# Kernel tuning notes

Measured on AMD Instinct MI355X. Metric: run time of the kernel, lower is better.

## Reference

```python
import jax, jax.numpy as jnp
import numpy as np


def _morpho(x, weight, bias, sign, padding, stride):
    # x: [B,C,H,W], weight: [B,C,kh,kw], bias: [B,C], sign: [B]
    B, C, H, W = x.shape
    kh, kw = weight.shape[-2:]
    # sign handling: if |sign| >= 1e-7 multiply by sign, else leave unchanged
    m = (jnp.abs(sign) >= 1e-7).astype(x.dtype)          # [B], constant (detached in torch)
    s = m * sign + (1.0 - m)                              # effective multiplier per sample
    xs = x * s[:, None, None, None]
    # unfold zero-pads, and sign*0 == 0, so padding signed x with zeros is equivalent
    xp = jnp.pad(xs, ((0, 0), (0, 0), (padding, padding), (padding, padding)))
    H2 = (H + 2 * padding - kh) // stride + 1
    W2 = (W + 2 * padding - kw) // stride + 1
    # direct windowed max-plus: y[b,c,i,j] = max_{p,q} xs_pad[b,c,i*s+p,j*s+q] + w[b,c,p,q]
    # small fixed kh*kw loop avoids materializing the B*C*kh*kw*L unfold tensor
    y = jnp.full((B, C, H2, W2), -jnp.inf, dtype=x.dtype)
    for p in range(kh):
        for q in range(kw):
            patch = jax.lax.slice(
                xp,
                (0, 0, p, q),
                (B, C, p + (H2 - 1) * stride + 1, q + (W2 - 1) * stride + 1),
                (1, 1, stride, stride),
            )  # [B,C,H2,W2]
            y = jnp.maximum(y, patch + weight[:, :, p, q][:, :, None, None])
    y = y + bias[:, :, None, None]
    return y * s[:, None, None, None]


def setup_inputs() -> dict:
    key = jax.random.key(0)
    k1, k2, k3, k4 = jax.random.split(key, 4)
    B, C, H, W, kh, kw = 16, 64, 128, 128, 5, 5
    return {
        "x": jax.random.normal(k1, (B, C, H, W), dtype=jnp.float32),
        "weight": jax.random.normal(k2, (B, C, kh, kw), dtype=jnp.float32) * 0.1,
        "bias": jax.random.normal(k3, (B, C), dtype=jnp.float32) * 0.1,
        "sign": jax.random.normal(k4, (B,), dtype=jnp.float32),
        "padding": 2,
        "stride": 1,
    }


def reference(x, weight, bias, sign, padding, stride):
    return _morpho(x, weight, bias, sign, padding, stride)
```

## Files before the change

### kernel.cpp

```cpp
#include <hip/hip_runtime.h>
#include <math.h>
#include <stdint.h>

#define HH 128
#define WW 128
#define NFLOATS (16 * 64 * HH * WW)

typedef __fp16 h2 __attribute__((ext_vector_type(2)));

__device__ __forceinline__ h2 h2max(h2 a, h2 b) { return __builtin_elementwise_max(a, b); }
__device__ __forceinline__ uint32_t h2u(h2 v) { return __builtin_bit_cast(uint32_t, v); }
__device__ __forceinline__ h2 uh2(uint32_t v) { return __builtin_bit_cast(h2, v); }

#if __has_builtin(__builtin_elementwise_fma)
#define H2FMA(a, b, c) __builtin_elementwise_fma((a), (b), (c))
#else
#define H2FMA(a, b, c) ((a) * (b) + (c))
#endif

__global__ __launch_bounds__(256, 8) void morpho_kernel(
    const float* __restrict__ x,
    const float* __restrict__ wgt,
    const float* __restrict__ bias,
    const float* __restrict__ sign,
    float* __restrict__ out)
{
    const int bid  = blockIdx.x;
    const int blk  = (bid & 7) * 512 + (bid >> 3);
    const int quad = blk & 3;
    const int bc   = blk >> 2;
    const int b    = bc >> 6;

    float*       __restrict__ yp = out + (size_t)bc * (HH * WW);
    const float* __restrict__ wp = wgt + bc * 25;

    const float sgn = sign[b];
    const float s   = (fabsf(sgn) >= 1e-7f) ? sgn : 1.0f;
    const float bvs = bias[bc] * s;
    const __fp16 sh = (__fp16)s;
    const h2 s2 = { sh, sh };

    uint32_t wsu[25];
#pragma unroll
    for (int k = 0; k < 25; ++k) {
        const __fp16 wh = (__fp16)wp[k];
        h2 w2 = { wh, wh };
        wsu[k] = (uint32_t)__builtin_amdgcn_readfirstlane((int)h2u(w2));
    }

    const int t  = threadIdx.x;
    const int tx = t & 31;
    const int ty = t >> 5;
    const int j0 = tx * 4;
    const int i0 = quad * 32 + ty * 4;
    const int planeOff = bc * (HH * WW);

    const bool mL = (tx > 0);
    const bool mR = (tx < 31);

    h2 acc0[4], acc1[4];

#pragma unroll
    for (int r8 = 0; r8 < 8; ++r8) {
        const int  r  = i0 - 2 + r8;
        const bool rv = ((unsigned)r < (unsigned)HH);
        const int  rc = min(max(r, 0), HH - 1);
        const int  oM = planeOff + rc * WW + j0;
        const int  oL = max(oM - 4, 0);
        const int  oR = min(oM + 4, NFLOATS - 4);
        const float4 v0 = *reinterpret_cast<const float4*>(x + oL);
        const float4 v1 = *reinterpret_cast<const float4*>(x + oM);
        const float4 v2 = *reinterpret_cast<const float4*>(x + oR);

        uint32_t e0 = h2u(__builtin_amdgcn_cvt_pkrtz(v0.z, v0.w));
        uint32_t e1 = h2u(__builtin_amdgcn_cvt_pkrtz(v1.x, v1.y));
        uint32_t e2 = h2u(__builtin_amdgcn_cvt_pkrtz(v1.z, v1.w));
        uint32_t e3 = h2u(__builtin_amdgcn_cvt_pkrtz(v2.x, v2.y));
        e0 = (rv && mL) ? e0 : 0u;
        e1 = rv ? e1 : 0u;
        e2 = rv ? e2 : 0u;
        e3 = (rv && mR) ? e3 : 0u;
        const uint32_t o0 = __builtin_amdgcn_alignbit(e1, e0, 16);
        const uint32_t o1 = __builtin_amdgcn_alignbit(e2, e1, 16);
        const uint32_t o2 = __builtin_amdgcn_alignbit(e3, e2, 16);

        const uint32_t P0[5] = { e0, o0, e1, o1, e2 };
        const uint32_t P1[5] = { e1, o1, e2, o2, e3 };

#pragma unroll
        for (int p = 0; p < 5; ++p) {
            const int oi = r8 - p;
            if (oi >= 0 && oi < 4) {
                const h2 w0 = uh2(wsu[p * 5 + 0]);
                const h2 w1 = uh2(wsu[p * 5 + 1]);
                const h2 w2 = uh2(wsu[p * 5 + 2]);
                const h2 w3 = uh2(wsu[p * 5 + 3]);
                const h2 w4 = uh2(wsu[p * 5 + 4]);
                {
                    const h2 t0 = H2FMA(uh2(P0[0]), s2, w0);
                    const h2 t1 = H2FMA(uh2(P0[1]), s2, w1);
                    const h2 t2 = H2FMA(uh2(P0[2]), s2, w2);
                    const h2 t3 = H2FMA(uh2(P0[3]), s2, w3);
                    const h2 t4 = H2FMA(uh2(P0[4]), s2, w4);
                    h2 mm = h2max(h2max(h2max(t0, t1), h2max(t2, t3)), t4);
                    acc0[oi] = (p == 0) ? mm : h2max(acc0[oi], mm);
                }
                {
                    const h2 t0 = H2FMA(uh2(P1[0]), s2, w0);
                    const h2 t1 = H2FMA(uh2(P1[1]), s2, w1);
                    const h2 t2 = H2FMA(uh2(P1[2]), s2, w2);
                    const h2 t3 = H2FMA(uh2(P1[3]), s2, w3);
                    const h2 t4 = H2FMA(uh2(P1[4]), s2, w4);
                    h2 mm = h2max(h2max(h2max(t0, t1), h2max(t2, t3)), t4);
                    acc1[oi] = (p == 0) ? mm : h2max(acc1[oi], mm);
                }
            }
        }
    }

#pragma unroll
    for (int a = 0; a < 4; ++a) {
        float4 o;
        o.x = fmaf((float)acc0[a][0], s, bvs);
        o.y = fmaf((float)acc0[a][1], s, bvs);
        o.z = fmaf((float)acc1[a][0], s, bvs);
        o.w = fmaf((float)acc1[a][1], s, bvs);
        *reinterpret_cast<float4*>(yp + (size_t)(i0 + a) * WW + j0) = o;
    }
}

extern "C" void kernel_launch(void* const* d_in, const int* in_sizes, int n_in,
                              void* d_out, int out_size, void* d_ws, size_t ws_size,
                              hipStream_t stream) {
    (void)d_ws; (void)ws_size; (void)in_sizes; (void)n_in; (void)out_size;
    const float* x    = (const float*)d_in[0];
    const float* w    = (const float*)d_in[1];
    const float* bias = (const float*)d_in[2];
    const float* sign = (const float*)d_in[3];
    float* out = (float*)d_out;

    morpho_kernel<<<4096, 256, 0, stream>>>(x, w, bias, sign, out);
}
```

Baseline: 33.54 us.

## Software-pipeline row loads with inline asm and explicit vmcnt waits

Replaces the compiler-scheduled row loop with hand-issued inline-asm global loads, kept four rows ahead, and explicit s_waitcnt vmcnt waits with sched barriers between consume steps. This overlaps memory latency with the packed-half max-plus math. The left and right halo loads shrink from float4 to float2, cutting redundant bytes. The launch-bounds occupancy hint of 8 is also dropped, which frees register pressure for the in-flight buffers but may lower occupancy.

```diff
diff --git a/kernel.cpp b/kernel.cpp
--- a/kernel.cpp
+++ b/kernel.cpp
@@ -18,7 +18,10 @@
 #define H2FMA(a, b, c) ((a) * (b) + (c))
 #endif
 
-__global__ __launch_bounds__(256, 8) void morpho_kernel(
+#define WAITV(n) do { asm volatile("s_waitcnt vmcnt(" #n ")" ::: "memory"); \
+                      __builtin_amdgcn_sched_barrier(0); } while (0)
+
+__global__ __launch_bounds__(256) void morpho_kernel(
     const float* __restrict__ x,
     const float* __restrict__ wgt,
     const float* __restrict__ bias,
@@ -54,28 +57,30 @@
     const int j0 = tx * 4;
     const int i0 = quad * 32 + ty * 4;
     const int planeOff = bc * (HH * WW);
-
     const bool mL = (tx > 0);
     const bool mR = (tx < 31);
 
+    float2 vl[8]; float4 vm[8]; float2 vr[8];
     h2 acc0[4], acc1[4];
 
-#pragma unroll
-    for (int r8 = 0; r8 < 8; ++r8) {
-        const int  r  = i0 - 2 + r8;
-        const bool rv = ((unsigned)r < (unsigned)HH);
-        const int  rc = min(max(r, 0), HH - 1);
-        const int  oM = planeOff + rc * WW + j0;
-        const int  oL = max(oM - 4, 0);
-        const int  oR = min(oM + 4, NFLOATS - 4);
-        const float4 v0 = *reinterpret_cast<const float4*>(x + oL);
-        const float4 v1 = *reinterpret_cast<const float4*>(x + oM);
-        const float4 v2 = *reinterpret_cast<const float4*>(x + oR);
+    auto ISSUE = [&](int r8) {
+        const int rrow = i0 - 2 + r8;
+        const int rc = min(max(rrow, 0), HH - 1);
+        const int oM = planeOff + rc * WW + j0;
+        const int oL = max(oM - 2, 0);
+        const int oR = min(oM + 4, NFLOATS - 2);
+        asm volatile("global_load_dwordx2 %0, %1, off" : "=v"(vl[r8]) : "v"(x + oL));
+        asm volatile("global_load_dwordx4 %0, %1, off" : "=v"(vm[r8]) : "v"(x + oM));
+        asm volatile("global_load_dwordx2 %0, %1, off" : "=v"(vr[r8]) : "v"(x + oR));
+    };
 
-        uint32_t e0 = h2u(__builtin_amdgcn_cvt_pkrtz(v0.z, v0.w));
-        uint32_t e1 = h2u(__builtin_amdgcn_cvt_pkrtz(v1.x, v1.y));
-        uint32_t e2 = h2u(__builtin_amdgcn_cvt_pkrtz(v1.z, v1.w));
-        uint32_t e3 = h2u(__builtin_amdgcn_cvt_pkrtz(v2.x, v2.y));
+    auto CONSUME = [&](int r8) {
+        const int  rrow = i0 - 2 + r8;
+        const bool rv = ((unsigned)rrow < (unsigned)HH);
+        uint32_t e0 = h2u(__builtin_amdgcn_cvt_pkrtz(vl[r8].x, vl[r8].y));
+        uint32_t e1 = h2u(__builtin_amdgcn_cvt_pkrtz(vm[r8].x, vm[r8].y));
+        uint32_t e2 = h2u(__builtin_amdgcn_cvt_pkrtz(vm[r8].z, vm[r8].w));
+        uint32_t e3 = h2u(__builtin_amdgcn_cvt_pkrtz(vr[r8].x, vr[r8].y));
         e0 = (rv && mL) ? e0 : 0u;
         e1 = rv ? e1 : 0u;
         e2 = rv ? e2 : 0u;
@@ -83,10 +88,8 @@
         const uint32_t o0 = __builtin_amdgcn_alignbit(e1, e0, 16);
         const uint32_t o1 = __builtin_amdgcn_alignbit(e2, e1, 16);
         const uint32_t o2 = __builtin_amdgcn_alignbit(e3, e2, 16);
-
         const uint32_t P0[5] = { e0, o0, e1, o1, e2 };
         const uint32_t P1[5] = { e1, o1, e2, o2, e3 };
-
 #pragma unroll
         for (int p = 0; p < 5; ++p) {
             const int oi = r8 - p;
@@ -116,7 +119,17 @@
                 }
             }
         }
-    }
+    };
+
+    ISSUE(0); ISSUE(1); ISSUE(2); ISSUE(3);
+    WAITV(9); CONSUME(0); ISSUE(4);
+    WAITV(9); CONSUME(1); ISSUE(5);
+    WAITV(9); CONSUME(2); ISSUE(6);
+    WAITV(9); CONSUME(3); ISSUE(7);
+    WAITV(9); CONSUME(4);
+    WAITV(6); CONSUME(5);
+    WAITV(3); CONSUME(6);
+    WAITV(0); CONSUME(7);
 
 #pragma unroll
     for (int a = 0; a < 4; ++a) {
```

After: 29.92 us. 1.12x faster.

## Replace halo loads with cross-lane shuffles and prefetch all rows via inline asm

Applied to the files above, without the earlier changes.

Each thread now loads only its own float4 per row instead of three overlapping float4s, and gets the left and right halo values from neighbouring lanes through shuffles. All eight row loads are issued up front with inline global_load asm, then consumed with staged vmcnt waits so compute on early rows overlaps later loads. The launch bounds occupancy hint is dropped. This cuts redundant global/L1 traffic but adds shuffle instructions and manual waitcnt handling, which may conflict with compiler scheduling.

```diff
diff --git a/kernel.cpp b/kernel.cpp
--- a/kernel.cpp
+++ b/kernel.cpp
@@ -4,7 +4,6 @@
 
 #define HH 128
 #define WW 128
-#define NFLOATS (16 * 64 * HH * WW)
 
 typedef __fp16 h2 __attribute__((ext_vector_type(2)));
 
@@ -18,7 +17,10 @@
 #define H2FMA(a, b, c) ((a) * (b) + (c))
 #endif
 
-__global__ __launch_bounds__(256, 8) void morpho_kernel(
+#define WAITV(n) do { asm volatile("s_waitcnt vmcnt(" #n ")" ::: "memory"); \
+                      __builtin_amdgcn_sched_barrier(0); } while (0)
+
+__global__ __launch_bounds__(256) void morpho_kernel(
     const float* __restrict__ x,
     const float* __restrict__ wgt,
     const float* __restrict__ bias,
@@ -54,36 +56,47 @@
     const int j0 = tx * 4;
     const int i0 = quad * 32 + ty * 4;
     const int planeOff = bc * (HH * WW);
-
     const bool mL = (tx > 0);
     const bool mR = (tx < 31);
+
+    asm volatile("s_waitcnt vmcnt(0)" ::: "memory");
+
+    float4 vm[8];
+#pragma unroll
+    for (int r8 = 0; r8 < 8; ++r8) {
+        const int rrow = i0 - 2 + r8;
+        const int rc   = min(max(rrow, 0), HH - 1);
+        const float* gp = x + planeOff + rc * WW + j0;
+        asm volatile("global_load_dwordx4 %0, %1, off" : "=v"(vm[r8]) : "v"(gp));
+    }
 
     h2 acc0[4], acc1[4];
 
 #pragma unroll
     for (int r8 = 0; r8 < 8; ++r8) {
-        const int  r  = i0 - 2 + r8;
-        const bool rv = ((unsigned)r < (unsigned)HH);
-        const int  rc = min(max(r, 0), HH - 1);
-        const int  oM = planeOff + rc * WW + j0;
-        const int  oL = max(oM - 4, 0);
-        const int  oR = min(oM + 4, NFLOATS - 4);
-        const float4 v0 = *reinterpret_cast<const float4*>(x + oL);
-        const float4 v1 = *reinterpret_cast<const float4*>(x + oM);
-        const float4 v2 = *reinterpret_cast<const float4*>(x + oR);
-
-        uint32_t e0 = h2u(__builtin_amdgcn_cvt_pkrtz(v0.z, v0.w));
-        uint32_t e1 = h2u(__builtin_amdgcn_cvt_pkrtz(v1.x, v1.y));
-        uint32_t e2 = h2u(__builtin_amdgcn_cvt_pkrtz(v1.z, v1.w));
-        uint32_t e3 = h2u(__builtin_amdgcn_cvt_pkrtz(v2.x, v2.y));
-        e0 = (rv && mL) ? e0 : 0u;
+        switch (7 - r8) {
+            case 7: WAITV(7); break;
+            case 6: WAITV(6); break;
+            case 5: WAITV(5); break;
+            case 4: WAITV(4); break;
+            case 3: WAITV(3); break;
+            case 2: WAITV(2); break;
+            case 1: WAITV(1); break;
+            default: WAITV(0); break;
+        }
+        const int  rrow = i0 - 2 + r8;
+        const bool rv = ((unsigned)rrow < (unsigned)HH);
+        uint32_t e1 = h2u(__builtin_amdgcn_cvt_pkrtz(vm[r8].x, vm[r8].y));
+        uint32_t e2 = h2u(__builtin_amdgcn_cvt_pkrtz(vm[r8].z, vm[r8].w));
         e1 = rv ? e1 : 0u;
         e2 = rv ? e2 : 0u;
-        e3 = (rv && mR) ? e3 : 0u;
+        uint32_t e0 = (uint32_t)__shfl_up((int)e2, 1, 32);
+        uint32_t e3 = (uint32_t)__shfl_down((int)e1, 1, 32);
+        e0 = mL ? e0 : 0u;
+        e3 = mR ? e3 : 0u;
         const uint32_t o0 = __builtin_amdgcn_alignbit(e1, e0, 16);
         const uint32_t o1 = __builtin_amdgcn_alignbit(e2, e1, 16);
         const uint32_t o2 = __builtin_amdgcn_alignbit(e3, e2, 16);
-
         const uint32_t P0[5] = { e0, o0, e1, o1, e2 };
         const uint32_t P1[5] = { e1, o1, e2, o2, e3 };
 
```

Result: faster. 27.93 us (-16.7%).
